# Kernel tuning notes

Measured on AMD Instinct MI355X. Metric: run time of the kernel, lower is better.

## Reference

```python
import jax, jax.numpy as jnp
import numpy as np

B, S, D = 4, 2048, 1024
KEY_DIM, VALUE_DIM = 1024, 1024
BETA = 1.0 / np.sqrt(D)  # beta defaults to 1/sqrt(input dim), per build()


def setup_inputs() -> dict:
    key = jax.random.key(0)
    ks = jax.random.split(key, 9)
    inv = 1.0 / np.sqrt(D)
    return {
        "query": jax.random.normal(ks[0], (B, S, D), dtype=jnp.float32),
        "key": jax.random.normal(ks[1], (B, S, D), dtype=jnp.float32),
        "value": jax.random.normal(ks[2], (B, S, D), dtype=jnp.float32),
        "Wq": jax.random.normal(ks[3], (D, KEY_DIM), dtype=jnp.float32) * inv,
        "bq": jnp.zeros((KEY_DIM,), dtype=jnp.float32),
        "Wk": jax.random.normal(ks[4], (D, KEY_DIM), dtype=jnp.float32) * inv,
        "bk": jnp.zeros((KEY_DIM,), dtype=jnp.float32),
        "Wv": jax.random.normal(ks[5], (D, VALUE_DIM), dtype=jnp.float32) * inv,
        "bv": jnp.zeros((VALUE_DIM,), dtype=jnp.float32),
    }


def reference(query, key, value, Wq, bq, Wk, bk, Wv, bv):
    # Dense projections
    q = query @ Wq + bq          # [B, S, key_dim]
    k = key @ Wk + bk            # [B, S, key_dim]
    v = value @ Wv + bv          # [B, S, value_dim]
    # Scaled dot-product attention (beta applied AFTER matmul, as in source)
    scores = jnp.einsum("bik,bjk->bij", q, k)  # [B, S, S]
    A = jax.nn.softmax(BETA * scores, axis=-1)
    return jnp.einsum("bij,bjk->bik", A, v)    # [B, S, value_dim]
```

## Files before the change

### kernel.cpp

```cpp
#include <hip/hip_runtime.h>


typedef __bf16 bf16x8 __attribute__((ext_vector_type(8)));
typedef float f32x4 __attribute__((ext_vector_type(4)));

#define MIB ((size_t)1 << 20)

__device__ __forceinline__ unsigned short f2b(float f) {
  unsigned int u = __float_as_uint(f);
  return (unsigned short)((u + 0x7FFFu + ((u >> 16) & 1u)) >> 16);
}

__device__ __forceinline__ void async16(const void* g, void* l) {
  __builtin_amdgcn_global_load_lds(
      (const __attribute__((address_space(1))) unsigned int*)g,
      (__attribute__((address_space(3))) unsigned int*)l, 16, 0, 0);
}

__device__ __forceinline__ unsigned ldsoff(const void* p) {
  return (unsigned)(size_t)(const __attribute__((address_space(3))) char*)p;
}

__device__ __forceinline__ bf16x8 ds_read16(unsigned off) {
  bf16x8 r;
  asm volatile("ds_read_b128 %0, %1" : "=v"(r) : "v"(off));
  return r;
}
__device__ __forceinline__ f32x4 ds_read16f(unsigned off) {
  f32x4 r;
  asm volatile("ds_read_b128 %0, %1" : "=v"(r) : "v"(off));
  return r;
}

__device__ __forceinline__ bf16x8 cvt8(f32x4 lo, f32x4 hi) {
  bf16x8 r;
  r[0] = (__bf16)lo[0]; r[1] = (__bf16)lo[1];
  r[2] = (__bf16)lo[2]; r[3] = (__bf16)lo[3];
  r[4] = (__bf16)hi[0]; r[5] = (__bf16)hi[1];
  r[6] = (__bf16)hi[2]; r[7] = (__bf16)hi[3];
  return r;
}

__device__ __forceinline__ void stage_tile_f32(
    const float* __restrict__ A, const unsigned short* __restrict__ Bt,
    char* dst, int K, int kb, int tid) {
#pragma unroll
  for (int i = 0; i < 8; ++i) {
    const int e = i * 256 + tid;
    const int r = e >> 4;
    const int cg = (e & 15) ^ ((r & 7) << 1);
    async16(A + (size_t)r * K + kb + cg * 4, dst + e * 16);
  }
#pragma unroll
  for (int i = 0; i < 4; ++i) {
    const int e = i * 256 + tid;
    const int r = e >> 3;
    const int cg = (e & 7) ^ (r & 7);
    async16(Bt + (size_t)r * K + kb + cg * 8, dst + 32768 + e * 16);
  }
}

template <bool SWAP>
__device__ __forceinline__ void gemm_loop_proj(
    const float* __restrict__ A, const unsigned short* __restrict__ Bt,
    char* lds, int K, int m0, int n0, f32x4 (&acc)[4][4]) {
  const int tid = threadIdx.x;
  const int lane = tid & 63;
  const int wave = tid >> 6;
  const int wm = (wave >> 1) * 64;
  const int wn = (wave & 1) * 64;
  const int fr = lane & 15;
  const int q = lane >> 4;
  const int NT = K >> 6;

  const float* Ab = A + (size_t)m0 * K;
  const unsigned short* Bb = Bt + (size_t)n0 * K;
  const unsigned LB = ldsoff(lds);

  unsigned oa[2][4], ob[2][4];
#pragma unroll
  for (int mi = 0; mi < 4; ++mi) {
    const int R = wm + mi * 16 + fr;
#pragma unroll
    for (int ks = 0; ks < 2; ++ks) {
      const int kc = ks * 4 + q;
      oa[ks][mi] = (unsigned)(R * 256 + (((2 * kc) ^ ((R & 7) << 1)) << 4));
    }
  }
#pragma unroll
  for (int ni = 0; ni < 4; ++ni) {
    const int R = wn + ni * 16 + fr;
#pragma unroll
    for (int ks = 0; ks < 2; ++ks) {
      const int kc = ks * 4 + q;
      ob[ks][ni] = (unsigned)(32768 + R * 128 + ((kc ^ (R & 7)) << 4));
    }
  }

  for (int t = 0; t < NT; ++t) {
    stage_tile_f32(Ab, Bb, lds, K, t << 6, tid);
    __syncthreads();

#pragma unroll
    for (int ks = 0; ks < 2; ++ks) {
      f32x4 alo[4], ahi[4];
      bf16x8 bv[4];
#pragma unroll
      for (int mi = 0; mi < 4; ++mi) {
        alo[mi] = ds_read16f(LB + oa[ks][mi]);
        ahi[mi] = ds_read16f(LB + oa[ks][mi] + 16);
      }
#pragma unroll
      for (int ni = 0; ni < 4; ++ni) bv[ni] = ds_read16(LB + ob[ks][ni]);

      asm volatile("s_waitcnt lgkmcnt(0)");
      __builtin_amdgcn_sched_barrier(0);

      bf16x8 av[4];
#pragma unroll
      for (int mi = 0; mi < 4; ++mi) av[mi] = cvt8(alo[mi], ahi[mi]);

#pragma unroll
      for (int mi = 0; mi < 4; ++mi)
#pragma unroll
        for (int ni = 0; ni < 4; ++ni)
          acc[mi][ni] = SWAP ? __builtin_amdgcn_mfma_f32_16x16x32_bf16(
                                   bv[ni], av[mi], acc[mi][ni], 0, 0, 0)
                             : __builtin_amdgcn_mfma_f32_16x16x32_bf16(
                                   av[mi], bv[ni], acc[mi][ni], 0, 0, 0);
    }
    __syncthreads();
  }
}

template <int TN>
__device__ __forceinline__ void stage_tile(
    const unsigned short* __restrict__ A, const unsigned short* __restrict__ Bt,
    unsigned short* dst, int K, int kb, int tid) {
#pragma unroll
  for (int i = 0; i < 4; ++i) {
    const int e = i * 256 + tid;
    const int r = e >> 3;
    const int cg = (e & 7) ^ (r & 7);
    async16(A + (size_t)r * K + kb + cg * 8, dst + e * 8);
  }
#pragma unroll
  for (int i = 0; i < TN / 32; ++i) {
    const int e = i * 256 + tid;
    const int r = e >> 3;
    const int cg = (e & 7) ^ (r & 7);
    async16(Bt + (size_t)r * K + kb + cg * 8, dst + 128 * 64 + e * 8);
  }
}

template <int TN, bool SWAP>
__device__ __forceinline__ void gemm_loop(
    const unsigned short* __restrict__ A, const unsigned short* __restrict__ Bt,
    unsigned short* lds, int K, int m0, int n0, f32x4 (&acc)[4][TN / 32]) {
  constexpr int NI = TN / 32;
  constexpr unsigned BUFB = (128 + TN) * 64 * 2;
  const int tid = threadIdx.x;
  const int lane = tid & 63;
  const int wave = tid >> 6;
  const int wm = (wave >> 1) * 64;
  const int wn = (wave & 1) * (TN / 2);
  const int fr = lane & 15;
  const int q = lane >> 4;
  const int NT = K >> 6;

  const unsigned short* Ab = A + (size_t)m0 * K;
  const unsigned short* Bb = Bt + (size_t)n0 * K;
  const unsigned LB = ldsoff(lds);

  unsigned oa[4][2], ob[NI][2];
#pragma unroll
  for (int mi = 0; mi < 4; ++mi) {
    const int R = wm + mi * 16 + fr;
#pragma unroll
    for (int ks = 0; ks < 2; ++ks) {
      const int kc = ks * 4 + q;
      oa[mi][ks] = (unsigned)((R * 64 + ((kc ^ (R & 7)) << 3)) * 2);
    }
  }
#pragma unroll
  for (int ni = 0; ni < NI; ++ni) {
    const int R = wn + ni * 16 + fr;
#pragma unroll
    for (int ks = 0; ks < 2; ++ks) {
      const int kc = ks * 4 + q;
      ob[ni][ks] =
          (unsigned)(128 * 64 * 2 + (R * 64 + ((kc ^ (R & 7)) << 3)) * 2);
    }
  }

  stage_tile<TN>(Ab, Bb, lds, K, 0, tid);
  __syncthreads();

  for (int t = 0; t < NT; ++t) {
    const unsigned boff = LB + (unsigned)(t & 1) * BUFB;
    if (t + 1 < NT)
      stage_tile<TN>(Ab, Bb, lds + ((t + 1) & 1) * (BUFB / 2), K,
                     (t + 1) << 6, tid);

    bf16x8 av[2][4], bv[2][NI];
#pragma unroll
    for (int ks = 0; ks < 2; ++ks)
#pragma unroll
      for (int mi = 0; mi < 4; ++mi) av[ks][mi] = ds_read16(boff + oa[mi][ks]);
#pragma unroll
    for (int ks = 0; ks < 2; ++ks)
#pragma unroll
      for (int ni = 0; ni < NI; ++ni) bv[ks][ni] = ds_read16(boff + ob[ni][ks]);

    asm volatile("s_waitcnt lgkmcnt(0)");
    __builtin_amdgcn_sched_barrier(0);

#pragma unroll
    for (int ks = 0; ks < 2; ++ks)
#pragma unroll
      for (int mi = 0; mi < 4; ++mi)
#pragma unroll
        for (int ni = 0; ni < NI; ++ni)
          acc[mi][ni] = SWAP ? __builtin_amdgcn_mfma_f32_16x16x32_bf16(
                                   bv[ks][ni], av[ks][mi], acc[mi][ni], 0, 0, 0)
                             : __builtin_amdgcn_mfma_f32_16x16x32_bf16(
                                   av[ks][mi], bv[ks][ni], acc[mi][ni], 0, 0, 0);

    __syncthreads();
  }
}

struct ProjArgs {
  const float* A[3];
  const unsigned short* Bt[3];
  unsigned short* C[3];
  const float* bias[3];
};

__global__ __launch_bounds__(256) void proj_qk(ProjArgs p) {
  __shared__ __align__(16) char lds[49152];
  const int z = blockIdx.z;
  const int m0 = blockIdx.y * 128;
  const int n0 = blockIdx.x * 128;

  f32x4 acc[4][4] = {};
  gemm_loop_proj<true>(p.A[z], p.Bt[z], lds, 1024, m0, n0, acc);

  const int lane = threadIdx.x & 63;
  const int wave = threadIdx.x >> 6;
  const int wm = (wave >> 1) * 64;
  const int wn = (wave & 1) * 64;
  const int fr = lane & 15;
  const int q4 = (lane >> 4) * 4;
  const float* bias = p.bias[z];
  unsigned short* C = p.C[z];

#pragma unroll
  for (int mi = 0; mi < 4; ++mi) {
    const int m = m0 + wm + mi * 16 + fr;
#pragma unroll
    for (int ni = 0; ni < 4; ++ni) {
      const int nb = n0 + wn + ni * 16 + q4;
      const float4 bb = *(const float4*)&bias[nb];
      ushort4 o = make_ushort4(
          f2b(acc[mi][ni][0] + bb.x), f2b(acc[mi][ni][1] + bb.y),
          f2b(acc[mi][ni][2] + bb.z), f2b(acc[mi][ni][3] + bb.w));
      *(ushort4*)&C[(size_t)m * 1024 + nb] = o;
    }
  }
}

__global__ __launch_bounds__(256) void proj_v(ProjArgs p) {
  __shared__ __align__(16) char lds[49152];
  const int m0 = blockIdx.y * 128;
  const int n0 = blockIdx.x * 128;

  f32x4 acc[4][4] = {};
  gemm_loop_proj<false>(p.A[2], p.Bt[2], lds, 1024, m0, n0, acc);

  const int lane = threadIdx.x & 63;
  const int wave = threadIdx.x >> 6;
  const int wm = (wave >> 1) * 64;
  const int wn = (wave & 1) * 64;
  const int fr = lane & 15;
  const int q4 = (lane >> 4) * 4;
  const float* bias = p.bias[2];

  unsigned short* C = p.C[2] + (size_t)(m0 >> 11) * (2048 * 1024);
#pragma unroll
  for (int mi = 0; mi < 4; ++mi) {
#pragma unroll
    for (int ni = 0; ni < 4; ++ni) {
      const int col = n0 + wn + ni * 16 + fr;
      const float bb = bias[col];
      const int rowb = (m0 + wm + mi * 16 + q4) & 2047;
      ushort4 o =
          make_ushort4(f2b(acc[mi][ni][0] + bb), f2b(acc[mi][ni][1] + bb),
                       f2b(acc[mi][ni][2] + bb), f2b(acc[mi][ni][3] + bb));
      *(ushort4*)&C[(size_t)col * 2048 + rowb] = o;
    }
  }
}

__global__ __launch_bounds__(256) void gemm_f32(
    const unsigned short* __restrict__ A, const unsigned short* __restrict__ Bt,
    float* __restrict__ C, int K, int ldc, long long sA, long long sB,
    long long sC) {
  __shared__ __align__(16) unsigned short lds[2 * 256 * 64];
  const int bz = blockIdx.z;
  A += (long long)bz * sA;
  Bt += (long long)bz * sB;
  C += (long long)bz * sC;
  const int m0 = blockIdx.y * 128;
  const int n0 = blockIdx.x * 128;

  f32x4 acc[4][4] = {};
  gemm_loop<128, true>(A, Bt, lds, K, m0, n0, acc);

  const int lane = threadIdx.x & 63;
  const int wave = threadIdx.x >> 6;
  const int wm = (wave >> 1) * 64;
  const int wn = (wave & 1) * 64;
  const int fr = lane & 15;
  const int q4 = (lane >> 4) * 4;
#pragma unroll
  for (int mi = 0; mi < 4; ++mi) {
    const int m = m0 + wm + mi * 16 + fr;
#pragma unroll
    for (int ni = 0; ni < 4; ++ni) {
      const int nb = n0 + wn + ni * 16 + q4;
      *(f32x4*)&C[(size_t)m * ldc + nb] = acc[mi][ni];
    }
  }
}

__global__ __launch_bounds__(256) void transpose3(
    const float* __restrict__ w0, const float* __restrict__ w1,
    const float* __restrict__ w2, unsigned short* __restrict__ t0,
    unsigned short* __restrict__ t1, unsigned short* __restrict__ t2) {
  __shared__ float t[32][33];
  const int K = 1024, N = 1024;
  const float* W = (blockIdx.z == 0) ? w0 : (blockIdx.z == 1) ? w1 : w2;
  unsigned short* WT = (blockIdx.z == 0) ? t0 : (blockIdx.z == 1) ? t1 : t2;
  const int n0 = blockIdx.x * 32, k0 = blockIdx.y * 32;
  const int tx = threadIdx.x, ty = threadIdx.y;
#pragma unroll
  for (int i = 0; i < 32; i += 8)
    t[ty + i][tx] = W[(size_t)(k0 + ty + i) * N + (n0 + tx)];
  __syncthreads();
#pragma unroll
  for (int i = 0; i < 32; i += 8)
    WT[(size_t)(n0 + ty + i) * K + (k0 + tx)] = f2b(t[tx][ty + i]);
}

__global__ __launch_bounds__(256) void softmax_rows(const float* __restrict__ S,
                                                    unsigned short* __restrict__ P) {
  const int cols = 2048;
  const size_t row = blockIdx.x;
  const float4* srow = (const float4*)(S + row * cols);
  const int tid = threadIdx.x;
  const int lane = tid & 63;
  const int wave = tid >> 6;

  float4 a = srow[tid];
  float4 b = srow[tid + 256];

  float mx = fmaxf(fmaxf(fmaxf(a.x, a.y), fmaxf(a.z, a.w)),
                   fmaxf(fmaxf(b.x, b.y), fmaxf(b.z, b.w)));
#pragma unroll
  for (int o = 1; o < 64; o <<= 1) mx = fmaxf(mx, __shfl_xor(mx, o));

  __shared__ float red[8];
  if (lane == 0) red[wave] = mx;
  __syncthreads();
  mx = fmaxf(fmaxf(red[0], red[1]), fmaxf(red[2], red[3]));

  const float c = 0.03125f * 1.4426950408889634f;
  float4 pa, pb;
  pa.x = exp2f((a.x - mx) * c); pa.y = exp2f((a.y - mx) * c);
  pa.z = exp2f((a.z - mx) * c); pa.w = exp2f((a.w - mx) * c);
  pb.x = exp2f((b.x - mx) * c); pb.y = exp2f((b.y - mx) * c);
  pb.z = exp2f((b.z - mx) * c); pb.w = exp2f((b.w - mx) * c);

  float sum = pa.x + pa.y + pa.z + pa.w + pb.x + pb.y + pb.z + pb.w;
#pragma unroll
  for (int o = 1; o < 64; o <<= 1) sum += __shfl_xor(sum, o);
  if (lane == 0) red[4 + wave] = sum;
  __syncthreads();
  sum = red[4] + red[5] + red[6] + red[7];

  const float inv = 1.0f / sum;
  ushort4* prow = (ushort4*)(P + row * cols);
  prow[tid] = make_ushort4(f2b(pa.x * inv), f2b(pa.y * inv), f2b(pa.z * inv),
                           f2b(pa.w * inv));
  prow[tid + 256] = make_ushort4(f2b(pb.x * inv), f2b(pb.y * inv),
                                 f2b(pb.z * inv), f2b(pb.w * inv));
}

extern "C" void kernel_launch(void* const* d_in, const int* in_sizes, int n_in,
                              void* d_out, int out_size, void* d_ws, size_t ws_size,
                              hipStream_t stream) {
  const float* query = (const float*)d_in[0];
  const float* key_ = (const float*)d_in[1];
  const float* value = (const float*)d_in[2];
  const float* Wq = (const float*)d_in[3];
  const float* bq = (const float*)d_in[4];
  const float* Wk = (const float*)d_in[5];
  const float* bk = (const float*)d_in[6];
  const float* Wv = (const float*)d_in[7];
  const float* bv = (const float*)d_in[8];
  float* out = (float*)d_out;

  char* ws = (char*)d_ws;
  unsigned short* WqT = (unsigned short*)ws;
  unsigned short* WkT = WqT + (size_t)1024 * 1024;
  unsigned short* WvT = WkT + (size_t)1024 * 1024;
  unsigned short* qb = (unsigned short*)(ws + 54 * MIB);
  unsigned short* kb = (unsigned short*)(ws + 70 * MIB);
  unsigned short* vT = (unsigned short*)(ws + 86 * MIB);
  float* sc = (float*)(ws + 102 * MIB);
  unsigned short* P = (unsigned short*)(ws + 6 * MIB);

  transpose3<<<dim3(32, 32, 3), dim3(32, 8), 0, stream>>>(Wq, Wk, Wv, WqT, WkT,
                                                          WvT);

  ProjArgs pa;
  pa.A[0] = query;  pa.A[1] = key_;  pa.A[2] = value;
  pa.Bt[0] = WqT; pa.Bt[1] = WkT; pa.Bt[2] = WvT;
  pa.C[0] = qb;  pa.C[1] = kb;  pa.C[2] = vT;
  pa.bias[0] = bq; pa.bias[1] = bk; pa.bias[2] = bv;

  proj_qk<<<dim3(8, 64, 2), 256, 0, stream>>>(pa);
  proj_v<<<dim3(8, 64, 1), 256, 0, stream>>>(pa);

  gemm_f32<<<dim3(16, 16, 4), 256, 0, stream>>>(
      qb, kb, sc, 1024, 2048, 2048LL * 1024, 2048LL * 1024, 2048LL * 2048);

  softmax_rows<<<8192, 256, 0, stream>>>(sc, P);

  gemm_f32<<<dim3(8, 16, 4), 256, 0, stream>>>(
      P, vT, out, 2048, 1024, 2048LL * 2048, 1024LL * 2048, 2048LL * 1024);
}
```

Before: 362.4 us.

## Double-buffer projection GEMM and convert fp32 A to bf16 before LDS

The projection GEMM loop now prefetches the next K-tile while computing the current one, using two LDS buffers. The fp32 activations are loaded into registers, converted to bf16 and written to LDS, so LDS holds half as many bytes and the per-MFMA conversion from fp32 LDS reads is removed. The B tile still uses async global-to-LDS loads into the alternate buffer. The cost is more registers held across the compute phase for the prefetched A data, which could reduce occupancy, plus a synchronous register-path load for A instead of async.

```diff
diff --git a/kernel.cpp b/kernel.cpp
--- a/kernel.cpp
+++ b/kernel.cpp
@@ -26,44 +26,11 @@
   asm volatile("ds_read_b128 %0, %1" : "=v"(r) : "v"(off));
   return r;
 }
-__device__ __forceinline__ f32x4 ds_read16f(unsigned off) {
-  f32x4 r;
-  asm volatile("ds_read_b128 %0, %1" : "=v"(r) : "v"(off));
-  return r;
-}
-
-__device__ __forceinline__ bf16x8 cvt8(f32x4 lo, f32x4 hi) {
-  bf16x8 r;
-  r[0] = (__bf16)lo[0]; r[1] = (__bf16)lo[1];
-  r[2] = (__bf16)lo[2]; r[3] = (__bf16)lo[3];
-  r[4] = (__bf16)hi[0]; r[5] = (__bf16)hi[1];
-  r[6] = (__bf16)hi[2]; r[7] = (__bf16)hi[3];
-  return r;
-}
-
-__device__ __forceinline__ void stage_tile_f32(
+
+template <bool SWAP>
+__device__ __forceinline__ void gemm_loop_projf(
     const float* __restrict__ A, const unsigned short* __restrict__ Bt,
-    char* dst, int K, int kb, int tid) {
-#pragma unroll
-  for (int i = 0; i < 8; ++i) {
-    const int e = i * 256 + tid;
-    const int r = e >> 4;
-    const int cg = (e & 15) ^ ((r & 7) << 1);
-    async16(A + (size_t)r * K + kb + cg * 4, dst + e * 16);
-  }
-#pragma unroll
-  for (int i = 0; i < 4; ++i) {
-    const int e = i * 256 + tid;
-    const int r = e >> 3;
-    const int cg = (e & 7) ^ (r & 7);
-    async16(Bt + (size_t)r * K + kb + cg * 8, dst + 32768 + e * 16);
-  }
-}
-
-template <bool SWAP>
-__device__ __forceinline__ void gemm_loop_proj(
-    const float* __restrict__ A, const unsigned short* __restrict__ Bt,
-    char* lds, int K, int m0, int n0, f32x4 (&acc)[4][4]) {
+    unsigned short* lds, int K, int m0, int n0, f32x4 (&acc)[4][4]) {
   const int tid = threadIdx.x;
   const int lane = tid & 63;
   const int wave = tid >> 6;
@@ -77,14 +44,14 @@
   const unsigned short* Bb = Bt + (size_t)n0 * K;
   const unsigned LB = ldsoff(lds);
 
-  unsigned oa[2][4], ob[2][4];
+  unsigned oa[4][2], ob[4][2];
 #pragma unroll
   for (int mi = 0; mi < 4; ++mi) {
     const int R = wm + mi * 16 + fr;
 #pragma unroll
     for (int ks = 0; ks < 2; ++ks) {
       const int kc = ks * 4 + q;
-      oa[ks][mi] = (unsigned)(R * 256 + (((2 * kc) ^ ((R & 7) << 1)) << 4));
+      oa[mi][ks] = (unsigned)((R * 64 + ((kc ^ (R & 7)) << 3)) * 2);
     }
   }
 #pragma unroll
@@ -93,42 +60,82 @@
 #pragma unroll
     for (int ks = 0; ks < 2; ++ks) {
       const int kc = ks * 4 + q;
-      ob[ks][ni] = (unsigned)(32768 + R * 128 + ((kc ^ (R & 7)) << 4));
-    }
-  }
+      ob[ni][ks] = (unsigned)(16384 + (R * 64 + ((kc ^ (R & 7)) << 3)) * 2);
+    }
+  }
+
+  float4 ar[4][2];
+  auto issueA = [&](int kb) {
+#pragma unroll
+    for (int i = 0; i < 4; ++i) {
+      const int e = i * 256 + tid;
+      const int r = e >> 3;
+      const int cg = (e & 7) ^ (r & 7);
+      const float* src = Ab + (size_t)r * K + kb + cg * 8;
+      ar[i][0] = *(const float4*)src;
+      ar[i][1] = *(const float4*)(src + 4);
+    }
+  };
+  auto issueB = [&](int kb, int buf) {
+#pragma unroll
+    for (int i = 0; i < 4; ++i) {
+      const int e = i * 256 + tid;
+      const int r = e >> 3;
+      const int cg = (e & 7) ^ (r & 7);
+      async16(Bb + (size_t)r * K + kb + cg * 8, lds + buf * 16384 + 8192 + e * 8);
+    }
+  };
+  auto writeA = [&](int buf) {
+#pragma unroll
+    for (int i = 0; i < 4; ++i) {
+      const int e = i * 256 + tid;
+      bf16x8 w;
+      w[0] = (__bf16)ar[i][0].x; w[1] = (__bf16)ar[i][0].y;
+      w[2] = (__bf16)ar[i][0].z; w[3] = (__bf16)ar[i][0].w;
+      w[4] = (__bf16)ar[i][1].x; w[5] = (__bf16)ar[i][1].y;
+      w[6] = (__bf16)ar[i][1].z; w[7] = (__bf16)ar[i][1].w;
+      *(bf16x8*)&lds[buf * 16384 + e * 8] = w;
+    }
+  };
+
+  issueA(0);
+  issueB(0, 0);
+  writeA(0);
+  __syncthreads();
 
   for (int t = 0; t < NT; ++t) {
-    stage_tile_f32(Ab, Bb, lds, K, t << 6, tid);
-    __syncthreads();
-
-#pragma unroll
-    for (int ks = 0; ks < 2; ++ks) {
-      f32x4 alo[4], ahi[4];
-      bf16x8 bv[4];
-#pragma unroll
-      for (int mi = 0; mi < 4; ++mi) {
-        alo[mi] = ds_read16f(LB + oa[ks][mi]);
-        ahi[mi] = ds_read16f(LB + oa[ks][mi] + 16);
-      }
-#pragma unroll
-      for (int ni = 0; ni < 4; ++ni) bv[ni] = ds_read16(LB + ob[ks][ni]);
-
-      asm volatile("s_waitcnt lgkmcnt(0)");
-      __builtin_amdgcn_sched_barrier(0);
-
-      bf16x8 av[4];
-#pragma unroll
-      for (int mi = 0; mi < 4; ++mi) av[mi] = cvt8(alo[mi], ahi[mi]);
-
+    const int cur = t & 1;
+    const unsigned boff = LB + (unsigned)cur * 32768;
+    if (t + 1 < NT) {
+      issueA((t + 1) << 6);
+      issueB((t + 1) << 6, cur ^ 1);
+    }
+
+    bf16x8 av[2][4], bv[2][4];
+#pragma unroll
+    for (int ks = 0; ks < 2; ++ks)
+#pragma unroll
+      for (int mi = 0; mi < 4; ++mi) av[ks][mi] = ds_read16(boff + oa[mi][ks]);
+#pragma unroll
+    for (int ks = 0; ks < 2; ++ks)
+#pragma unroll
+      for (int ni = 0; ni < 4; ++ni) bv[ks][ni] = ds_read16(boff + ob[ni][ks]);
+
+    asm volatile("s_waitcnt lgkmcnt(0)");
+    __builtin_amdgcn_sched_barrier(0);
+
+#pragma unroll
+    for (int ks = 0; ks < 2; ++ks)
 #pragma unroll
       for (int mi = 0; mi < 4; ++mi)
 #pragma unroll
         for (int ni = 0; ni < 4; ++ni)
           acc[mi][ni] = SWAP ? __builtin_amdgcn_mfma_f32_16x16x32_bf16(
-                                   bv[ni], av[mi], acc[mi][ni], 0, 0, 0)
+                                   bv[ks][ni], av[ks][mi], acc[mi][ni], 0, 0, 0)
                              : __builtin_amdgcn_mfma_f32_16x16x32_bf16(
-                                   av[mi], bv[ni], acc[mi][ni], 0, 0, 0);
-    }
+                                   av[ks][mi], bv[ks][ni], acc[mi][ni], 0, 0, 0);
+
+    if (t + 1 < NT) writeA(cur ^ 1);
     __syncthreads();
   }
 }
@@ -238,13 +245,13 @@
 };
 
 __global__ __launch_bounds__(256) void proj_qk(ProjArgs p) {
-  __shared__ __align__(16) char lds[49152];
+  __shared__ __align__(16) unsigned short lds[2 * 16384];
   const int z = blockIdx.z;
   const int m0 = blockIdx.y * 128;
   const int n0 = blockIdx.x * 128;
 
   f32x4 acc[4][4] = {};
-  gemm_loop_proj<true>(p.A[z], p.Bt[z], lds, 1024, m0, n0, acc);
+  gemm_loop_projf<true>(p.A[z], p.Bt[z], lds, 1024, m0, n0, acc);
 
   const int lane = threadIdx.x & 63;
   const int wave = threadIdx.x >> 6;
@@ -271,12 +278,12 @@
 }
 
 __global__ __launch_bounds__(256) void proj_v(ProjArgs p) {
-  __shared__ __align__(16) char lds[49152];
+  __shared__ __align__(16) unsigned short lds[2 * 16384];
   const int m0 = blockIdx.y * 128;
   const int n0 = blockIdx.x * 128;
 
   f32x4 acc[4][4] = {};
-  gemm_loop_proj<false>(p.A[2], p.Bt[2], lds, 1024, m0, n0, acc);
+  gemm_loop_projf<false>(p.A[2], p.Bt[2], lds, 1024, m0, n0, acc);
 
   const int lane = threadIdx.x & 63;
   const int wave = threadIdx.x >> 6;
```

Measured after the change: 363.5 us. About the same (+0.3%).
